# Optimization experiments

Hardware: AMD Instinct MI355X
Metric: run time of the kernel (lower is better)

Reference implementation:

```python
import jax, jax.numpy as jnp
import numpy as np

B = 32768          # batch
SEQ, F = 128, 8    # input_seq_len_samples, num_features
D = SEQ * F        # flattened input dim = 1024
E = 16             # num_experts
H1 = 256           # expert hidden
H2 = H1 // 2       # 128
GH = 128           # gating hidden


def _init_linear(key, fan_in, shape_w, shape_b):
    # torch nn.Linear default: U(-1/sqrt(fan_in), 1/sqrt(fan_in))
    kw, kb = jax.random.split(key)
    lim = 1.0 / np.sqrt(fan_in)
    W = jax.random.uniform(kw, shape_w, jnp.float32, -lim, lim)
    b = jax.random.uniform(kb, shape_b, jnp.float32, -lim, lim)
    return W, b


def setup_inputs() -> dict:
    key = jax.random.key(0)
    ks = jax.random.split(key, 6)
    x = jax.random.normal(ks[0], (B, SEQ, F), jnp.float32)
    # stacked expert weights: [E, in, out] layout
    W1, b1 = _init_linear(ks[1], D, (E, D, H1), (E, H1))
    W2, b2 = _init_linear(ks[2], H1, (E, H1, H2), (E, H2))
    W3, b3 = _init_linear(ks[3], H2, (E, H2, 1), (E, 1))
    Wg1, bg1 = _init_linear(ks[4], D, (D, GH), (GH,))
    Wg2, bg2 = _init_linear(ks[5], GH, (GH, E), (E,))
    return {"x": x, "W1": W1, "b1": b1, "W2": W2, "b2": b2,
            "W3": W3, "b3": b3, "Wg1": Wg1, "bg1": bg1,
            "Wg2": Wg2, "bg2": bg2}


def reference(x, W1, b1, W2, b2, W3, b3, Wg1, bg1, Wg2, bg2):
    bsz = x.shape[0]
    flat_x = x.reshape(bsz, -1)                      # [B, D]
    # gating network
    g = jax.nn.relu(flat_x @ Wg1 + bg1)              # [B, GH]
    gating_logits = g @ Wg2 + bg2                    # [B, E]
    gating_weights = jax.nn.softmax(gating_logits, axis=1)
    # all experts as one batched GEMM stack
    h = jax.nn.relu(jnp.einsum('bd,edh->beh', flat_x, W1) + b1)   # [B,E,H1]
    h = jax.nn.relu(jnp.einsum('beh,ehk->bek', h, W2) + b2)       # [B,E,H2]
    expert_outputs = jnp.einsum('bek,eko->beo', h, W3) + b3       # [B,E,1]
    final_output = jnp.sum(gating_weights[:, :, None] * expert_outputs, axis=1)  # [B,1]
    return final_output, gating_weights
```

## Files before the change

### kernel.cpp

```cpp
#include <hip/hip_runtime.h>
#include <stdint.h>
#include <stddef.h>

typedef short bf16x8 __attribute__((ext_vector_type(8)));
typedef float f32x4 __attribute__((ext_vector_type(4)));

__device__ __forceinline__ unsigned short bf16rn(float f){
  unsigned int u = __builtin_bit_cast(unsigned int, f);
  u += 0x7fffu + ((u >> 16) & 1u);
  return (unsigned short)(u >> 16);
}

__device__ __forceinline__ void gll16(const void* gsrc, void* ldst){
  __builtin_amdgcn_global_load_lds((const __attribute__((address_space(1))) unsigned int*)gsrc,
                                   (__attribute__((address_space(3))) unsigned int*)ldst,
                                   16, 0, 0);
}

__device__ __forceinline__ void barfence(){
  asm volatile("" ::: "memory");
  __builtin_amdgcn_s_barrier();
  asm volatile("" ::: "memory");
}

__global__ __launch_bounds__(256) void k_cvt_x(const float* __restrict__ x,
                                               unsigned short* __restrict__ xb, long n){
  long i = ((long)blockIdx.x * blockDim.x + threadIdx.x) * 8;
  if (i >= n) return;
  const float4* p = (const float4*)(x + i);
  float4 a = p[0], b = p[1];
  union { unsigned short h[8]; uint4 u; } r;
  r.h[0]=bf16rn(a.x); r.h[1]=bf16rn(a.y); r.h[2]=bf16rn(a.z); r.h[3]=bf16rn(a.w);
  r.h[4]=bf16rn(b.x); r.h[5]=bf16rn(b.y); r.h[6]=bf16rn(b.z); r.h[7]=bf16rn(b.w);
  *(uint4*)(xb + i) = r.u;
}

__global__ __launch_bounds__(256) void k_cvt_w(const float* __restrict__ src,
                                               unsigned short* __restrict__ dst,
                                               int K, int N){
  __shared__ float t[32][33];
  int e = blockIdx.z, k0 = blockIdx.x * 32, n0 = blockIdx.y * 32;
  const float* s = src + (size_t)e * K * N;
  unsigned short* d = dst + (size_t)e * N * K;
  int tx = threadIdx.x, ty = threadIdx.y;
  #pragma unroll
  for (int j = 0; j < 4; j++)
    t[ty + j*8][tx] = s[(size_t)(k0 + ty + j*8) * N + n0 + tx];
  __syncthreads();
  #pragma unroll
  for (int j = 0; j < 4; j++){
    int n = ty + j*8;
    d[(size_t)(n0 + n) * K + k0 + tx] = bf16rn(t[tx][n]);
  }
}

__global__ __launch_bounds__(128) void k_gating(const unsigned short* __restrict__ xb,
                                                const unsigned short* __restrict__ wg1t,
                                                const float* __restrict__ bg1,
                                                const float* __restrict__ wg2,
                                                const float* __restrict__ bg2,
                                                float* __restrict__ gout, int chunk_base){
  __shared__ unsigned short As[32*64];
  __shared__ unsigned short Bs[128*64];
  __shared__ float gl[32][129];
  __shared__ float redg[32][17];
  const int t = threadIdx.x, wid = t >> 6, l = t & 63;
  const int m0 = blockIdx.x * 32;
  const int jb = l & 7, rsub = l >> 3;
  f32x4 acc[2][4];
  #pragma unroll
  for (int i=0;i<2;i++)
    #pragma unroll
    for (int j=0;j<4;j++) acc[i][j] = (f32x4)0.f;

  for (int kt = 0; kt < 16; kt++){
    int k0 = kt * 64;
    #pragma unroll
    for (int i = 0; i < 2; i++){
      int idx = wid*2 + i; int row = idx*8 + rsub;
      gll16(xb + (size_t)(m0 + row)*1024 + k0 + ((jb ^ (row & 7)) << 3), As + idx*512);
    }
    #pragma unroll
    for (int i = 0; i < 8; i++){
      int idx = wid*8 + i; int row = idx*8 + rsub;
      gll16(wg1t + (size_t)row*1024 + k0 + ((jb ^ (row & 7)) << 3), Bs + idx*512);
    }
    __syncthreads();
    #pragma unroll
    for (int ks = 0; ks < 2; ks++){
      int blk = ks*4 + (l >> 4);
      bf16x8 a[2], b[4];
      #pragma unroll
      for (int fi = 0; fi < 2; fi++){
        int r = fi*16 + (l & 15);
        a[fi] = *(const bf16x8*)(As + r*64 + ((blk ^ (r & 7)) << 3));
      }
      #pragma unroll
      for (int fj = 0; fj < 4; fj++){
        int r = wid*64 + fj*16 + (l & 15);
        b[fj] = *(const bf16x8*)(Bs + r*64 + ((blk ^ (r & 7)) << 3));
      }
      #pragma unroll
      for (int fi = 0; fi < 2; fi++)
        #pragma unroll
        for (int fj = 0; fj < 4; fj++)
          acc[fi][fj] = __builtin_amdgcn_mfma_f32_16x16x32_bf16(a[fi], b[fj], acc[fi][fj], 0, 0, 0);
    }
    __syncthreads();
  }
  #pragma unroll
  for (int fi = 0; fi < 2; fi++)
    #pragma unroll
    for (int fj = 0; fj < 4; fj++){
      int c = wid*64 + fj*16 + (l & 15);
      float bv = bg1[c];
      #pragma unroll
      for (int r = 0; r < 4; r++){
        int row = fi*16 + (l >> 4)*4 + r;
        float v = acc[fi][fj][r] + bv;
        gl[row][c] = v > 0.f ? v : 0.f;
      }
    }
  __syncthreads();

  {
    const int row = t & 31, kq = t >> 5;
    float p[16];
    #pragma unroll
    for (int e = 0; e < 16; e++) p[e] = 0.f;
    for (int k = kq*32; k < kq*32 + 32; k++){
      float g = gl[row][k];
      const float* w = wg2 + k*16;
      #pragma unroll
      for (int e = 0; e < 16; e++) p[e] += g * w[e];
    }
    #pragma unroll
    for (int e = 0; e < 16; e++) p[e] += __shfl_xor(p[e], 32);
    if (t >= 64 && t < 96){
      #pragma unroll
      for (int e = 0; e < 16; e++) redg[t - 64][e] = p[e];
    }
    __syncthreads();
    if (t < 32){
      float le[16];
      #pragma unroll
      for (int e = 0; e < 16; e++) le[e] = bg2[e] + p[e] + redg[t][e];
      float m = le[0];
      #pragma unroll
      for (int e = 1; e < 16; e++) m = fmaxf(m, le[e]);
      float s = 0.f;
      #pragma unroll
      for (int e = 0; e < 16; e++){ le[e] = __expf(le[e] - m); s += le[e]; }
      float inv = 1.f / s;
      float4* o = (float4*)(gout + (size_t)(chunk_base + m0 + t)*16);
      #pragma unroll
      for (int q = 0; q < 4; q++)
        o[q] = make_float4(le[4*q]*inv, le[4*q+1]*inv, le[4*q+2]*inv, le[4*q+3]*inv);
    }
  }
}

template<int I0, int J0>
__device__ __forceinline__ void mfma_quad(const bf16x8 (&A)[4][2], const bf16x8 (&Bv)[2][2],
                                          f32x4 (&acc)[8][4]){
  #pragma unroll
  for (int fi = 0; fi < 4; ++fi)
    #pragma unroll
    for (int ks = 0; ks < 2; ++ks){
      acc[I0+fi][J0]   = __builtin_amdgcn_mfma_f32_16x16x32_bf16(A[fi][ks], Bv[0][ks], acc[I0+fi][J0],   0,0,0);
      acc[I0+fi][J0+1] = __builtin_amdgcn_mfma_f32_16x16x32_bf16(A[fi][ks], Bv[1][ks], acc[I0+fi][J0+1], 0,0,0);
    }
}

__global__ __launch_bounds__(512, 2) void k_fused(const unsigned short* __restrict__ xb,
                                                  const unsigned short* __restrict__ w1t,
                                                  const float* __restrict__ b1,
                                                  const unsigned short* __restrict__ w2t,
                                                  const float* __restrict__ b2,
                                                  const float* __restrict__ w3,
                                                  const float* __restrict__ b3,
                                                  float* __restrict__ outE,
                                                  int chunkB){
  extern __shared__ __align__(16) char smem[];
  const int t = threadIdx.x;
  const int wid = t >> 6, l = t & 63;
  const int wrow = wid >> 2, wcol = wid & 3;
  const int l3 = l >> 3, l7 = l & 7, l15 = l & 15, l4 = l >> 4;

  const int bid = blockIdx.x;
  const int slot = bid >> 3;
  const int e = (bid & 7)*2 + (slot & 1);
  const int mt = slot >> 1;
  const int m0 = mt * 256, n0 = e * 256;

  auto STAGE = [&](int isB, int p, int h, int kt){
    const unsigned short* gb = isB ? (w1t + (size_t)(n0 + h*128) * 1024)
                                   : (xb  + (size_t)(m0 + h*128) * 1024);
    char* dbase = smem + ((p << 16) | (isB << 15) | (h << 14));
    #pragma unroll
    for (int j = 0; j < 2; j++){
      int r = j*64 + wid*8 + l3;
      size_t src = (size_t)r * 1024 + (size_t)kt*64 + (size_t)((l7 ^ (r & 7)) << 3);
      gll16(gb + src, dbase + j*8192 + wid*1024);
    }
  };
  auto LDA = [&](int p, int qm, int fi, int ks) -> bf16x8 {
    int row = qm*64 + fi*16 + l15;
    int kb = (((ks << 2) | l4) ^ (row & 7)) << 4;
    return *(const bf16x8*)(smem + (p << 16) + (wrow << 14) + row*128 + kb);
  };
  auto LDB = [&](int p, int qn, int fj, int ks) -> bf16x8 {
    int row = (wcol & 1)*64 + qn*32 + fj*16 + l15;
    int kb = (((ks << 2) | l4) ^ (row & 7)) << 4;
    return *(const bf16x8*)(smem + (p << 16) + 32768 + ((wcol >> 1) << 14) + row*128 + kb);
  };

  f32x4 acc[8][4];
  #pragma unroll
  for (int i = 0; i < 8; i++)
    #pragma unroll
    for (int j = 0; j < 4; j++) acc[i][j] = (f32x4)0.f;

  bf16x8 a0[4][2], a1[4][2], b0[2][2], b1v[2][2];

  STAGE(0,0,0,0); STAGE(1,0,0,0); STAGE(0,0,1,0); STAGE(1,0,1,0);
  STAGE(1,1,0,1); STAGE(0,1,0,1);
  asm volatile("s_waitcnt vmcnt(4)" ::: "memory");
  barfence();

  for (int it = 0; it < 8; ++it){
    const int t0 = 2*it, k1 = t0 + 1;
    int c2 = t0 + 2, c3 = t0 + 3;
    if (c2 > 15) c2 = 14;
    if (c3 > 15) c3 = 14;

    #pragma unroll
    for (int fi = 0; fi < 4; ++fi){ a0[fi][0] = LDA(0,0,fi,0); a0[fi][1] = LDA(0,0,fi,1); }
    #pragma unroll
    for (int fj = 0; fj < 2; ++fj){ b0[fj][0] = LDB(0,0,fj,0); b0[fj][1] = LDB(0,0,fj,1); }
    STAGE(1,1,1,k1);
    barfence();
    __builtin_amdgcn_s_setprio(1);
    mfma_quad<0,0>(a0, b0, acc);
    __builtin_amdgcn_s_setprio(0);
    barfence();

    #pragma unroll
    for (int fj = 0; fj < 2; ++fj){ b1v[fj][0] = LDB(0,1,fj,0); b1v[fj][1] = LDB(0,1,fj,1); }
    STAGE(0,1,1,k1);
    barfence();
    __builtin_amdgcn_s_setprio(1);
    mfma_quad<0,2>(a0, b1v, acc);
    __builtin_amdgcn_s_setprio(0);
    barfence();

    #pragma unroll
    for (int fi = 0; fi < 4; ++fi){ a1[fi][0] = LDA(0,1,fi,0); a1[fi][1] = LDA(0,1,fi,1); }
    STAGE(1,0,0,c2);
    barfence();
    __builtin_amdgcn_s_setprio(1);
    mfma_quad<4,2>(a1, b1v, acc);
    __builtin_amdgcn_s_setprio(0);
    barfence();

    STAGE(0,0,0,c2);
    barfence();
    __builtin_amdgcn_s_setprio(1);
    mfma_quad<4,0>(a1, b0, acc);
    __builtin_amdgcn_s_setprio(0);
    asm volatile("s_waitcnt vmcnt(4)" ::: "memory");
    barfence();

    #pragma unroll
    for (int fi = 0; fi < 4; ++fi){ a0[fi][0] = LDA(1,0,fi,0); a0[fi][1] = LDA(1,0,fi,1); }
    #pragma unroll
    for (int fj = 0; fj < 2; ++fj){ b0[fj][0] = LDB(1,0,fj,0); b0[fj][1] = LDB(1,0,fj,1); }
    STAGE(1,0,1,c2);
    barfence();
    __builtin_amdgcn_s_setprio(1);
    mfma_quad<0,0>(a0, b0, acc);
    __builtin_amdgcn_s_setprio(0);
    barfence();

    #pragma unroll
    for (int fj = 0; fj < 2; ++fj){ b1v[fj][0] = LDB(1,1,fj,0); b1v[fj][1] = LDB(1,1,fj,1); }
    STAGE(0,0,1,c2);
    barfence();
    __builtin_amdgcn_s_setprio(1);
    mfma_quad<0,2>(a0, b1v, acc);
    __builtin_amdgcn_s_setprio(0);
    barfence();

    #pragma unroll
    for (int fi = 0; fi < 4; ++fi){ a1[fi][0] = LDA(1,1,fi,0); a1[fi][1] = LDA(1,1,fi,1); }
    STAGE(1,1,0,c3);
    barfence();
    __builtin_amdgcn_s_setprio(1);
    mfma_quad<4,2>(a1, b1v, acc);
    __builtin_amdgcn_s_setprio(0);
    barfence();

    STAGE(0,1,0,c3);
    barfence();
    __builtin_amdgcn_s_setprio(1);
    mfma_quad<4,0>(a1, b0, acc);
    __builtin_amdgcn_s_setprio(0);
    asm volatile("s_waitcnt vmcnt(4)" ::: "memory");
    barfence();
  }

  __syncthreads();

  {
    float bv[4];
    #pragma unroll
    for (int fj = 0; fj < 4; ++fj) bv[fj] = b1[e*256 + wcol*64 + fj*16 + l15];
    #pragma unroll
    for (int fi = 0; fi < 8; ++fi)
      #pragma unroll
      for (int fj = 0; fj < 4; ++fj){
        const int col = wcol*64 + fj*16 + l15;
        #pragma unroll
        for (int r = 0; r < 4; ++r){
          const int row = wrow*128 + fi*16 + l4*4 + r;
          float v = acc[fi][fj][r] + bv[fj];
          v = v > 0.f ? v : 0.f;
          *(unsigned short*)(smem + row*512 + ((((col >> 3) ^ (row & 31))) << 4) + ((col & 7) << 1)) = bf16rn(v);
        }
      }
  }

  const unsigned short* w2e = w2t + (size_t)e*(128*256);
  auto STAGE_W2 = [&](int c, int q){
    char* dbase = smem + 131072 + q*16384;
    #pragma unroll
    for (int j = 0; j < 2; j++){
      int r = j*64 + wid*8 + l3;
      size_t src = (size_t)r*256 + (size_t)c*64 + (size_t)((l7 ^ (r & 7)) << 3);
      gll16(w2e + src, dbase + j*8192 + wid*1024);
    }
  };
  STAGE_W2(0, 0);
  __syncthreads();

  const int wr2 = wid >> 1, wc2 = wid & 1;
  f32x4 acc2[4][4];
  #pragma unroll
  for (int i = 0; i < 4; i++)
    #pragma unroll
    for (int j = 0; j < 4; j++) acc2[i][j] = (f32x4)0.f;

  float w3v[4], b2v[4];
  #pragma unroll
  for (int fj = 0; fj < 4; ++fj){
    int c = wc2*64 + fj*16 + l15;
    w3v[fj] = w3[e*128 + c];
    b2v[fj] = b2[e*128 + c];
  }

  for (int c = 0; c < 4; ++c){
    if (c < 3) STAGE_W2(c+1, (c+1)&1);
    bf16x8 a2[4][2], bb[4][2];
    #pragma unroll
    for (int fi = 0; fi < 4; ++fi)
      #pragma unroll
      for (int ks = 0; ks < 2; ++ks){
        int row = wr2*64 + fi*16 + l15;
        int sl = (c*8 + ks*4 + l4) ^ (row & 31);
        a2[fi][ks] = *(const bf16x8*)(smem + row*512 + (sl << 4));
      }
    #pragma unroll
    for (int fj = 0; fj < 4; ++fj)
      #pragma unroll
      for (int ks = 0; ks < 2; ++ks){
        int n = wc2*64 + fj*16 + l15;
        int sl = (ks*4 + l4) ^ (n & 7);
        bb[fj][ks] = *(const bf16x8*)(smem + 131072 + (c&1)*16384 + n*128 + (sl << 4));
      }
    __builtin_amdgcn_s_setprio(1);
    #pragma unroll
    for (int fi = 0; fi < 4; ++fi)
      #pragma unroll
      for (int fj = 0; fj < 4; ++fj)
        #pragma unroll
        for (int ks = 0; ks < 2; ++ks)
          acc2[fi][fj] = __builtin_amdgcn_mfma_f32_16x16x32_bf16(a2[fi][ks], bb[fj][ks], acc2[fi][fj], 0, 0, 0);
    __builtin_amdgcn_s_setprio(0);
    __syncthreads();
  }

  float* red = (float*)(smem + 131072);
  #pragma unroll
  for (int fi = 0; fi < 4; ++fi)
    #pragma unroll
    for (int r = 0; r < 4; ++r){
      float s = 0.f;
      #pragma unroll
      for (int fj = 0; fj < 4; ++fj){
        float v = acc2[fi][fj][r] + b2v[fj];
        v = v > 0.f ? v : 0.f;
        s += v * w3v[fj];
      }
      s += __shfl_xor(s, 1); s += __shfl_xor(s, 2);
      s += __shfl_xor(s, 4); s += __shfl_xor(s, 8);
      if (l15 == 0){
        int row = wr2*64 + fi*16 + l4*4 + r;
        red[row*2 + wc2] = s;
      }
    }
  __syncthreads();
  if (t < 256)
    outE[(size_t)e*chunkB + m0 + t] = red[t*2 + 0] + red[t*2 + 1] + b3[e];
}

__global__ __launch_bounds__(256) void k_stage2b(const float* __restrict__ outE,
                                                 float* __restrict__ dout,
                                                 int chunk_base, int chunkB, int Btot){
  int row = blockIdx.x*256 + threadIdx.x;
  int rowg = chunk_base + row;
  const float* g = dout + Btot + (size_t)rowg*16;
  float s = 0.f;
  #pragma unroll
  for (int e = 0; e < 16; e++) s += g[e] * outE[(size_t)e*chunkB + row];
  dout[rowg] = s;
}

extern "C" void kernel_launch(void* const* d_in, const int* in_sizes, int n_in,
                              void* d_out, int out_size, void* d_ws, size_t ws_size,
                              hipStream_t stream){
  const float* x   = (const float*)d_in[0];
  const float* W1  = (const float*)d_in[1];
  const float* b1  = (const float*)d_in[2];
  const float* W2  = (const float*)d_in[3];
  const float* b2  = (const float*)d_in[4];
  const float* W3  = (const float*)d_in[5];
  const float* b3  = (const float*)d_in[6];
  const float* Wg1 = (const float*)d_in[7];
  const float* bg1 = (const float*)d_in[8];
  const float* Wg2 = (const float*)d_in[9];
  const float* bg2 = (const float*)d_in[10];
  float* out = (float*)d_out;

  const int B = in_sizes[0] / 1024;

  char* ws = (char*)d_ws;
  size_t off = 0;
  auto alloc = [&](size_t bytes){ size_t p = off; off = (off + bytes + 255) & ~(size_t)255; return p; };
  size_t o_w1t  = alloc((size_t)16*256*1024*2);
  size_t o_w2t  = alloc((size_t)16*128*256*2);
  size_t o_wg1t = alloc((size_t)128*1024*2);
  size_t fixed = off;

  const int cands[6] = {1, 2, 4, 8, 16, 32};
  int nc = 32;
  for (int i = 0; i < 6; i++){
    size_t cB = (size_t)B / cands[i];
    if (fixed + cB*2112 + 4096 <= ws_size){ nc = cands[i]; break; }
  }
  int chunkB = B / nc;

  size_t o_xb = alloc((size_t)chunkB*1024*2);
  size_t o_oe = alloc((size_t)chunkB*16*4);

  unsigned short* w1t  = (unsigned short*)(ws + o_w1t);
  unsigned short* w2t  = (unsigned short*)(ws + o_w2t);
  unsigned short* wg1t = (unsigned short*)(ws + o_wg1t);
  unsigned short* xb   = (unsigned short*)(ws + o_xb);
  float*          oE   = (float*)(ws + o_oe);

  hipFuncSetAttribute(reinterpret_cast<const void*>(k_fused),
                      hipFuncAttributeMaxDynamicSharedMemorySize, 163840);

  k_cvt_w<<<dim3(32, 8, 16), dim3(32, 8), 0, stream>>>(W1, w1t, 1024, 256);
  k_cvt_w<<<dim3(8, 4, 16),  dim3(32, 8), 0, stream>>>(W2, w2t, 256, 128);
  k_cvt_w<<<dim3(32, 4, 1),  dim3(32, 8), 0, stream>>>(Wg1, wg1t, 1024, 128);

  for (int c = 0; c < nc; c++){
    int cb = c * chunkB;
    k_cvt_x<<<chunkB/2, 256, 0, stream>>>(x + (size_t)cb*1024, xb, (long)chunkB*1024);
    k_gating<<<chunkB/32, 128, 0, stream>>>(xb, wg1t, bg1, Wg2, bg2, out + B, cb);
    k_fused<<<chunkB/16, 512, 163840, stream>>>(xb, w1t, b1, w2t, b2, W3, b3, oE, chunkB);
    k_stage2b<<<chunkB/256, 256, 0, stream>>>(oE, out, cb, chunkB, B);
  }
}
```

Measured before the change: 366.7 us.

## Fuse x bf16 conversion into gating kernel and read W2 directly from global

```diff
diff --git a/kernel.cpp b/kernel.cpp
--- a/kernel.cpp
+++ b/kernel.cpp
@@ -21,18 +21,6 @@
   asm volatile("" ::: "memory");
   __builtin_amdgcn_s_barrier();
   asm volatile("" ::: "memory");
-}
-
-__global__ __launch_bounds__(256) void k_cvt_x(const float* __restrict__ x,
-                                               unsigned short* __restrict__ xb, long n){
-  long i = ((long)blockIdx.x * blockDim.x + threadIdx.x) * 8;
-  if (i >= n) return;
-  const float4* p = (const float4*)(x + i);
-  float4 a = p[0], b = p[1];
-  union { unsigned short h[8]; uint4 u; } r;
-  r.h[0]=bf16rn(a.x); r.h[1]=bf16rn(a.y); r.h[2]=bf16rn(a.z); r.h[3]=bf16rn(a.w);
-  r.h[4]=bf16rn(b.x); r.h[5]=bf16rn(b.y); r.h[6]=bf16rn(b.z); r.h[7]=bf16rn(b.w);
-  *(uint4*)(xb + i) = r.u;
 }
 
 __global__ __launch_bounds__(256) void k_cvt_w(const float* __restrict__ src,
@@ -54,7 +42,8 @@
   }
 }
 
-__global__ __launch_bounds__(128) void k_gating(const unsigned short* __restrict__ xb,
+__global__ __launch_bounds__(128) void k_gating(const float* __restrict__ x,
+                                                unsigned short* __restrict__ xb,
                                                 const unsigned short* __restrict__ wg1t,
                                                 const float* __restrict__ bg1,
                                                 const float* __restrict__ wg2,
@@ -77,8 +66,15 @@
     int k0 = kt * 64;
     #pragma unroll
     for (int i = 0; i < 2; i++){
-      int idx = wid*2 + i; int row = idx*8 + rsub;
-      gll16(xb + (size_t)(m0 + row)*1024 + k0 + ((jb ^ (row & 7)) << 3), As + idx*512);
+      int s = t + i*128;
+      int row = s >> 3, sk = s & 7;
+      const float4* px = (const float4*)(x + (size_t)(m0 + row)*1024 + k0 + sk*8);
+      float4 u0 = px[0], u1 = px[1];
+      union { unsigned short h[8]; uint4 u; bf16x8 v; } r;
+      r.h[0]=bf16rn(u0.x); r.h[1]=bf16rn(u0.y); r.h[2]=bf16rn(u0.z); r.h[3]=bf16rn(u0.w);
+      r.h[4]=bf16rn(u1.x); r.h[5]=bf16rn(u1.y); r.h[6]=bf16rn(u1.z); r.h[7]=bf16rn(u1.w);
+      *(bf16x8*)(As + row*64 + ((sk ^ (row & 7)) << 3)) = r.v;
+      *(uint4*)(xb + (size_t)(m0 + row)*1024 + k0 + sk*8) = r.u;
     }
     #pragma unroll
     for (int i = 0; i < 8; i++){
@@ -329,20 +325,9 @@
         }
       }
   }
+  __syncthreads();
 
   const unsigned short* w2e = w2t + (size_t)e*(128*256);
-  auto STAGE_W2 = [&](int c, int q){
-    char* dbase = smem + 131072 + q*16384;
-    #pragma unroll
-    for (int j = 0; j < 2; j++){
-      int r = j*64 + wid*8 + l3;
-      size_t src = (size_t)r*256 + (size_t)c*64 + (size_t)((l7 ^ (r & 7)) << 3);
-      gll16(w2e + src, dbase + j*8192 + wid*1024);
-    }
-  };
-  STAGE_W2(0, 0);
-  __syncthreads();
-
   const int wr2 = wid >> 1, wc2 = wid & 1;
   f32x4 acc2[4][4];
   #pragma unroll
@@ -358,8 +343,8 @@
     b2v[fj] = b2[e*128 + c];
   }
 
+  #pragma unroll
   for (int c = 0; c < 4; ++c){
-    if (c < 3) STAGE_W2(c+1, (c+1)&1);
     bf16x8 a2[4][2], bb[4][2];
     #pragma unroll
     for (int fi = 0; fi < 4; ++fi)
@@ -374,8 +359,7 @@
       #pragma unroll
       for (int ks = 0; ks < 2; ++ks){
         int n = wc2*64 + fj*16 + l15;
-        int sl = (ks*4 + l4) ^ (n & 7);
-        bb[fj][ks] = *(const bf16x8*)(smem + 131072 + (c&1)*16384 + n*128 + (sl << 4));
+        bb[fj][ks] = *(const bf16x8*)(w2e + (size_t)n*256 + c*64 + ks*32 + l4*8);
       }
     __builtin_amdgcn_s_setprio(1);
     #pragma unroll
@@ -386,7 +370,6 @@
         for (int ks = 0; ks < 2; ++ks)
           acc2[fi][fj] = __builtin_amdgcn_mfma_f32_16x16x32_bf16(a2[fi][ks], bb[fj][ks], acc2[fi][fj], 0, 0, 0);
     __builtin_amdgcn_s_setprio(0);
-    __syncthreads();
   }
 
   float* red = (float*)(smem + 131072);
@@ -477,8 +460,7 @@
 
   for (int c = 0; c < nc; c++){
     int cb = c * chunkB;
-    k_cvt_x<<<chunkB/2, 256, 0, stream>>>(x + (size_t)cb*1024, xb, (long)chunkB*1024);
-    k_gating<<<chunkB/32, 128, 0, stream>>>(xb, wg1t, bg1, Wg2, bg2, out + B, cb);
+    k_gating<<<chunkB/32, 128, 0, stream>>>(x + (size_t)cb*1024, xb, wg1t, bg1, Wg2, bg2, out + B, cb);
     k_fused<<<chunkB/16, 512, 163840, stream>>>(xb, w1t, b1, w2t, b2, W3, b3, oE, chunkB);
     k_stage2b<<<chunkB/256, 256, 0, stream>>>(oE, out, cb, chunkB, B);
   }
```

Measured after the change: 375.3 us. 2.3% more time.
